# Optimization experiments

Measured on AMD Instinct MI355X. Metric: run time of the kernel, lower is better.

The kernel has to match this reference:

```python
import jax, jax.numpy as jnp
import numpy as np

NUM_NODES = 100000
NUM_EDGES = 1600000
IN_DIM = 128
HID = 128
OUT_DIM = 5


def setup_inputs() -> dict:
    key = jax.random.key(0)
    ks = jax.random.split(key, 8)
    x = jax.random.normal(ks[0], (NUM_NODES, IN_DIM), dtype=jnp.float32)
    edges = jax.random.randint(ks[1], (2, NUM_EDGES), 0, NUM_NODES, dtype=jnp.int32)
    s = 1.0 / np.sqrt(IN_DIM)
    W1 = jax.random.uniform(ks[2], (IN_DIM, HID), jnp.float32, -s, s)
    b1 = jax.random.uniform(ks[3], (HID,), jnp.float32, -s, s)
    sh = 1.0 / np.sqrt(HID)
    W2 = jax.random.uniform(ks[4], (HID, HID), jnp.float32, -sh, sh)
    b2 = jax.random.uniform(ks[5], (HID,), jnp.float32, -sh, sh)
    Wp = jax.random.uniform(ks[6], (HID, OUT_DIM), jnp.float32, -sh, sh)
    bp = jax.random.uniform(ks[7], (OUT_DIM,), jnp.float32, -sh, sh)
    return {"x": x, "edges": edges, "W1": W1, "b1": b1, "W2": W2, "b2": b2, "Wp": Wp, "bp": bp}


def _gnn_layer(x, src, tgt, W, b):
    # scatter-add of source features into targets (mean aggregation)
    agg = jax.ops.segment_sum(x[src], tgt, num_segments=NUM_NODES)  # [N, d]
    cnt = jax.ops.segment_sum(jnp.ones_like(tgt, dtype=x.dtype), tgt, num_segments=NUM_NODES)
    cnt = jnp.maximum(cnt, 1.0)  # clamp(min=1)
    agg = agg / cnt[:, None]
    combined = x + agg  # residual
    return jax.nn.relu(combined @ W + b)


def reference(x, edges, W1, b1, W2, b2, Wp, bp):
    src, tgt = edges[0], edges[1]
    h = _gnn_layer(x, src, tgt, W1, b1)
    h = _gnn_layer(h, src, tgt, W2, b2)
    return h @ Wp + bp  # [N, OUT_DIM]
```

## Files before the change

kernel.cpp:

```cpp
#include <hip/hip_runtime.h>

typedef unsigned int uint32;
typedef unsigned short ushort16;

typedef __attribute__((ext_vector_type(8))) short short8;
typedef __attribute__((ext_vector_type(4))) float f32x4;

#define BMAX 512


__device__ __forceinline__ ushort16 f2bf(float f) {
    uint32 u = __float_as_uint(f);
    u += 0x7fffu + ((u >> 16) & 1u);
    return (ushort16)(u >> 16);
}
__device__ __forceinline__ float bfhi(uint32 u) { return __uint_as_float(u & 0xffff0000u); }
__device__ __forceinline__ float bflo(uint32 u) { return __uint_as_float(u << 16); }
__device__ __forceinline__ uint32 pack2(float a, float b) {
    return (uint32)f2bf(a) | ((uint32)f2bf(b) << 16);
}

union U16 { uint4 u; short8 s; };
__device__ __forceinline__ short8 ld_frag(const ushort16* p) {
    U16 x; x.u = *(const uint4*)p; return x.s;
}

#define ACC8(v) \
    acc[0] += bflo(v.x); acc[1] += bfhi(v.x); \
    acc[2] += bflo(v.y); acc[3] += bfhi(v.y); \
    acc[4] += bflo(v.z); acc[5] += bfhi(v.z); \
    acc[6] += bflo(v.w); acc[7] += bfhi(v.w);

__device__ __forceinline__ void bucket_scan(const int* __restrict__ total, int B,
                                            int* bs , int* sd ) {
    int tid = threadIdx.x;
    int v0 = (2 * tid     < B) ? total[2 * tid]     : 0;
    int v1 = (2 * tid + 1 < B) ? total[2 * tid + 1] : 0;
    int s = v0 + v1;
    sd[tid] = s;
    __syncthreads();
    for (int o = 1; o < 256; o <<= 1) {
        int t = (tid >= o) ? sd[tid - o] : 0;
        __syncthreads();
        sd[tid] += t;
        __syncthreads();
    }
    int excl = sd[tid] - s;
    bs[2 * tid]     = excl;
    bs[2 * tid + 1] = excl + v0;
    __syncthreads();
}

__global__ __launch_bounds__(256)
void hist_cvt_prep_kernel(const int* __restrict__ tgt, int* __restrict__ hist,
                          const float* __restrict__ x, uint4* __restrict__ xb,
                          const float* __restrict__ W1, const float* __restrict__ W2,
                          ushort16* __restrict__ Wt1, ushort16* __restrict__ Wt2,
                          int E, int C, int B, int G1, int n64) {
    int tid = threadIdx.x, blk = blockIdx.x;
    if (blk >= G1) {
        const float* W = (blk - G1) ? W2 : W1;
        ushort16* Wt = (blk - G1) ? Wt2 : Wt1;
        for (int i = tid; i < 16384; i += 256) {
            int k = i >> 7, c = i & 127;
            Wt[c * 128 + k] = f2bf(W[i]);
        }
        return;
    }
    __shared__ int lh[BMAX];
    for (int b = tid; b < B; b += 256) lh[b] = 0;
    __syncthreads();
    int q0 = blk * (C / 4), q1 = min(q0 + C / 4, E / 4);
    for (int q = q0 + tid; q < q1; q += 256) {
        int4 t = ((const int4*)tgt)[q];
        atomicAdd(&lh[t.x >> 8], 1);
        atomicAdd(&lh[t.y >> 8], 1);
        atomicAdd(&lh[t.z >> 8], 1);
        atomicAdd(&lh[t.w >> 8], 1);
    }
    if (blk == 0 && tid == 0) {
        for (int e = (E / 4) * 4; e < E; ++e) atomicAdd(&lh[tgt[e] >> 8], 1);
    }
    for (int i = blk * 256 + tid; i < n64; i += G1 * 256) {
        const float4* p = (const float4*)x + (size_t)i * 16;
        uint4* q = xb + (size_t)i * 8;
#pragma unroll
        for (int j = 0; j < 8; ++j) {
            float4 a = p[2 * j], bb = p[2 * j + 1];
            uint4 o;
            o.x = pack2(a.x, a.y); o.y = pack2(a.z, a.w);
            o.z = pack2(bb.x, bb.y); o.w = pack2(bb.z, bb.w);
            q[j] = o;
        }
    }
    __syncthreads();
    for (int b = tid; b < B; b += 256) hist[blk * B + b] = lh[b];
}

__global__ __launch_bounds__(256)
void colscan_kernel(int* __restrict__ hist, int* __restrict__ total, int G1, int B) {
    __shared__ int sd[256];
    __shared__ int carrySh;
    int b = blockIdx.x, tid = threadIdx.x;
    if (tid == 0) carrySh = 0;
    __syncthreads();
    for (int g0 = 0; g0 < G1; g0 += 256) {
        int g = g0 + tid;
        int v = (g < G1) ? hist[g * B + b] : 0;
        int c0 = carrySh;
        sd[tid] = v;
        __syncthreads();
        for (int o = 1; o < 256; o <<= 1) {
            int t = (tid >= o) ? sd[tid - o] : 0;
            __syncthreads();
            sd[tid] += t;
            __syncthreads();
        }
        if (g < G1) hist[g * B + b] = sd[tid] - v + c0;
        int tot = sd[255];
        __syncthreads();
        if (tid == 0) carrySh = c0 + tot;
        __syncthreads();
    }
    if (tid == 0) total[b] = carrySh;
}

__global__ __launch_bounds__(256)
void partition_kernel(const int* __restrict__ src, const int* __restrict__ tgt,
                      const int* __restrict__ hist, const int* __restrict__ total,
                      uint32* __restrict__ ebuf, int E, int C, int B) {
    __shared__ int bs[512];
    __shared__ int sd[256];
    __shared__ int cur[BMAX];
    int tid = threadIdx.x, blk = blockIdx.x;
    bucket_scan(total, B, bs, sd);
    for (int b = tid; b < B; b += 256) cur[b] = hist[blk * B + b] + bs[b];
    __syncthreads();
    int q0 = blk * (C / 4), q1 = min(q0 + C / 4, E / 4);
    for (int q = q0 + tid; q < q1; q += 256) {
        int4 t = ((const int4*)tgt)[q];
        int4 s = ((const int4*)src)[q];
        int p0 = atomicAdd(&cur[t.x >> 8], 1);
        int p1 = atomicAdd(&cur[t.y >> 8], 1);
        int p2 = atomicAdd(&cur[t.z >> 8], 1);
        int p3 = atomicAdd(&cur[t.w >> 8], 1);
        ebuf[p0] = ((uint32)(t.x & 255) << 24) | (uint32)s.x;
        ebuf[p1] = ((uint32)(t.y & 255) << 24) | (uint32)s.y;
        ebuf[p2] = ((uint32)(t.z & 255) << 24) | (uint32)s.z;
        ebuf[p3] = ((uint32)(t.w & 255) << 24) | (uint32)s.w;
    }
    if (blk == 0 && tid == 0) {
        for (int e = (E / 4) * 4; e < E; ++e) {
            int t = tgt[e], s = src[e];
            int p = atomicAdd(&cur[t >> 8], 1);
            ebuf[p] = ((uint32)(t & 255) << 24) | (uint32)s;
        }
    }
}

__global__ __launch_bounds__(256)
void csr_kernel(const uint32* __restrict__ ebuf, const int* __restrict__ total,
                int* __restrict__ offsets, int* __restrict__ csr, int N, int B, int E) {
    __shared__ int bs[512];
    __shared__ int sd[256];
    __shared__ int cnt[256];
    int b = blockIdx.x, tid = threadIdx.x;
    bucket_scan(total, B, bs, sd);
    int s = bs[b];
    int n = bs[b + 1] - s;
    int t0 = b << 8;
    cnt[tid] = 0;
    __syncthreads();
    {
        int a0 = (s + 3) & ~3, a1 = (s + n) & ~3;
        for (int i = s + tid; i < min(a0, s + n); i += 256) atomicAdd(&cnt[ebuf[i] >> 24], 1);
        for (int q = a0 / 4 + tid; q < a1 / 4; q += 256) {
            uint4 e4 = ((const uint4*)ebuf)[q];
            atomicAdd(&cnt[e4.x >> 24], 1);
            atomicAdd(&cnt[e4.y >> 24], 1);
            atomicAdd(&cnt[e4.z >> 24], 1);
            atomicAdd(&cnt[e4.w >> 24], 1);
        }
        for (int i = max(a1, s) + tid; i < s + n; i += 256) atomicAdd(&cnt[ebuf[i] >> 24], 1);
    }
    __syncthreads();
    int v = cnt[tid];
    sd[tid] = v;
    __syncthreads();
    for (int o = 1; o < 256; o <<= 1) {
        int t = (tid >= o) ? sd[tid - o] : 0;
        __syncthreads();
        sd[tid] += t;
        __syncthreads();
    }
    int excl = sd[tid] - v;
    int t = t0 + tid;
    if (t < N) offsets[t] = s + excl;
    if (b == B - 1 && tid == 255) offsets[N] = E;
    __syncthreads();
    cnt[tid] = s + excl;
    __syncthreads();
    for (int i = tid; i < n; i += 256) {
        uint32 e = ebuf[s + i];
        int slot = atomicAdd(&cnt[e >> 24], 1);
        csr[slot] = (int)(e & 0x00FFFFFFu);
    }
}

__global__ __launch_bounds__(256, 4)
void agg_combine_bf16_kernel(const ushort16* __restrict__ hb,
                             const int* __restrict__ offsets, const int* __restrict__ csr,
                             uint32* __restrict__ outb, int N) {
    int wid = (blockIdx.x * 256 + threadIdx.x) >> 6;
    int lane = threadIdx.x & 63;
    if (wid >= N) return;
    int g = lane >> 4, sl = lane & 15;
    int s0 = offsets[wid];
    int deg = offsets[wid + 1] - s0;
    int fi = sl * 4 + g;
    uint32 su = ((const uint32*)hb)[(size_t)wid * 64 + fi];

    float acc[8];
#pragma unroll
    for (int j = 0; j < 8; ++j) acc[j] = 0.f;

    int base = 0;
    for (; base + 8 <= deg; base += 8) {
        int i0 = csr[s0 + base + g];
        int i1 = csr[s0 + base + 4 + g];
        uint4 v0 = *(const uint4*)(hb + (size_t)i0 * 128 + sl * 8);
        uint4 v1 = *(const uint4*)(hb + (size_t)i1 * 128 + sl * 8);
        ACC8(v0); ACC8(v1);
    }
    for (; base < deg; base += 4) {
        int e = base + g;
        if (e < deg) {
            int s = csr[s0 + e];
            uint4 v = *(const uint4*)(hb + (size_t)s * 128 + sl * 8);
            ACC8(v);
        }
    }
#pragma unroll
    for (int j = 0; j < 8; ++j) {
        acc[j] += __shfl_xor(acc[j], 16, 64);
        acc[j] += __shfl_xor(acc[j], 32, 64);
    }
    float inv = 1.f / fmaxf((float)deg, 1.f);
    float ax = (g == 0) ? acc[0] : (g == 1) ? acc[2] : (g == 2) ? acc[4] : acc[6];
    float ay = (g == 0) ? acc[1] : (g == 1) ? acc[3] : (g == 2) ? acc[5] : acc[7];
    outb[(size_t)wid * 64 + fi] = pack2(bflo(su) + ax * inv, bfhi(su) + ay * inv);
}

__global__ __launch_bounds__(256)
void gemm_mfma_kernel(const ushort16* __restrict__ A, const ushort16* __restrict__ Wt,
                      const float* __restrict__ bias, int M,
                      ushort16* __restrict__ outB,
                      const float* __restrict__ Wp, const float* __restrict__ bp,
                      float* __restrict__ outP) {
    const int tid = threadIdx.x;
    const int lane = tid & 63;
    const int wave = tid >> 6;
    const int l15 = lane & 15;
    const int quad = lane >> 4;
    const int r0 = blockIdx.x * 64 + wave * 16;

    int arow = r0 + l15;
    if (arow >= M) arow = M - 1;
    const ushort16* aptr = A + (size_t)arow * 128 + quad * 8;
    short8 afr[4];
#pragma unroll
    for (int kt = 0; kt < 4; ++kt) afr[kt] = ld_frag(aptr + kt * 32);

    f32x4 acc[8];
#pragma unroll
    for (int t = 0; t < 8; ++t) acc[t] = (f32x4){0.f, 0.f, 0.f, 0.f};

#pragma unroll
    for (int t = 0; t < 8; ++t) {
        const ushort16* bptr = Wt + (size_t)(16 * t + l15) * 128 + quad * 8;
        short8 b0 = ld_frag(bptr);
        short8 b1 = ld_frag(bptr + 32);
        short8 b2 = ld_frag(bptr + 64);
        short8 b3 = ld_frag(bptr + 96);
        acc[t] = __builtin_amdgcn_mfma_f32_16x16x32_bf16(afr[0], b0, acc[t], 0, 0, 0);
        acc[t] = __builtin_amdgcn_mfma_f32_16x16x32_bf16(afr[1], b1, acc[t], 0, 0, 0);
        acc[t] = __builtin_amdgcn_mfma_f32_16x16x32_bf16(afr[2], b2, acc[t], 0, 0, 0);
        acc[t] = __builtin_amdgcn_mfma_f32_16x16x32_bf16(afr[3], b3, acc[t], 0, 0, 0);
    }

    if (outP) {
        float p[4][5];
#pragma unroll
        for (int r = 0; r < 4; ++r)
#pragma unroll
            for (int j = 0; j < 5; ++j) p[r][j] = 0.f;
#pragma unroll
        for (int t = 0; t < 8; ++t) {
            float wpl[5];
#pragma unroll
            for (int j = 0; j < 5; ++j) wpl[j] = Wp[(16 * t + l15) * 5 + j];
            float bt = bias[16 * t + l15];
            float ov[4];
            ov[0] = fmaxf(acc[t].x + bt, 0.f);
            ov[1] = fmaxf(acc[t].y + bt, 0.f);
            ov[2] = fmaxf(acc[t].z + bt, 0.f);
            ov[3] = fmaxf(acc[t].w + bt, 0.f);
#pragma unroll
            for (int r = 0; r < 4; ++r)
#pragma unroll
                for (int j = 0; j < 5; ++j) p[r][j] += ov[r] * wpl[j];
        }
#pragma unroll
        for (int m = 1; m <= 8; m <<= 1)
#pragma unroll
            for (int r = 0; r < 4; ++r)
#pragma unroll
                for (int j = 0; j < 5; ++j) p[r][j] += __shfl_xor(p[r][j], m, 64);
        if (l15 == 0) {
#pragma unroll
            for (int r = 0; r < 4; ++r) {
                int row = r0 + quad * 4 + r;
                if (row < M) {
#pragma unroll
                    for (int j = 0; j < 5; ++j) outP[(size_t)row * 5 + j] = p[r][j] + bp[j];
                }
            }
        }
    } else {
#pragma unroll
        for (int t = 0; t < 8; ++t) {
            float bt = bias[16 * t + l15];
            float ov[4];
            ov[0] = fmaxf(acc[t].x + bt, 0.f);
            ov[1] = fmaxf(acc[t].y + bt, 0.f);
            ov[2] = fmaxf(acc[t].z + bt, 0.f);
            ov[3] = fmaxf(acc[t].w + bt, 0.f);
#pragma unroll
            for (int r = 0; r < 4; ++r) {
                float nb = __shfl_xor(ov[r], 1, 64);
                int row = r0 + quad * 4 + r;
                if (((l15 & 1) == 0) && row < M) {
                    *(uint32*)(outB + (size_t)row * 128 + 16 * t + l15) = pack2(ov[r], nb);
                }
            }
        }
    }
}

extern "C" void kernel_launch(void* const* d_in, const int* in_sizes, int n_in,
                              void* d_out, int out_size, void* d_ws, size_t ws_size,
                              hipStream_t stream) {
    const float* x     = (const float*)d_in[0];
    const int*   edges = (const int*)d_in[1];
    const float* W1    = (const float*)d_in[2];
    const float* b1    = (const float*)d_in[3];
    const float* W2    = (const float*)d_in[4];
    const float* b2    = (const float*)d_in[5];
    const float* Wp    = (const float*)d_in[6];
    const float* bp    = (const float*)d_in[7];
    float* out = (float*)d_out;

    const int N = in_sizes[0] / 128;
    const int E = in_sizes[1] / 2;
    const int* src = edges;
    const int* tgt = edges + E;

    const int B  = (N + 255) >> 8;
    const int C  = 4096;
    const int G1 = (E + C - 1) / C;
    const int n64 = N * 2;

    char* ws = (char*)d_ws;
    size_t off = 0;
    auto alloc = [&](size_t bytes) {
        char* p = ws + off;
        off = (off + bytes + 255) & ~(size_t)255;
        return p;
    };
    int*      offsets = (int*)alloc((size_t)(N + 1) * 4);
    int*      csr     = (int*)alloc((size_t)E * 4);
    ushort16* xb      = (ushort16*)alloc((size_t)N * 128 * 2);
    ushort16* hb1     = (ushort16*)alloc((size_t)N * 128 * 2);
    ushort16* bufAb   = (ushort16*)alloc((size_t)N * 128 * 2);
    ushort16* Wt1     = (ushort16*)alloc(128 * 128 * 2);
    ushort16* Wt2     = (ushort16*)alloc(128 * 128 * 2);
    int*      hist    = (int*)alloc((size_t)G1 * B * 4);
    int*      total   = (int*)alloc((size_t)B * 4);
    uint32*   ebuf    = (uint32*)bufAb;
    (void)ws_size;

    hist_cvt_prep_kernel<<<G1 + 2, 256, 0, stream>>>(tgt, hist, x, (uint4*)xb,
                                                     W1, W2, Wt1, Wt2, E, C, B, G1, n64);
    colscan_kernel<<<B, 256, 0, stream>>>(hist, total, G1, B);
    partition_kernel<<<G1, 256, 0, stream>>>(src, tgt, hist, total, ebuf, E, C, B);
    csr_kernel<<<B, 256, 0, stream>>>(ebuf, total, offsets, csr, N, B, E);

    const int aggBlocks  = (N + 3) / 4;
    const int gemmBlocks = (N + 63) / 64;

    agg_combine_bf16_kernel<<<aggBlocks, 256, 0, stream>>>(xb, offsets, csr, (uint32*)bufAb, N);
    gemm_mfma_kernel<<<gemmBlocks, 256, 0, stream>>>(bufAb, Wt1, b1, N, hb1,
                                                     nullptr, nullptr, nullptr);
    agg_combine_bf16_kernel<<<aggBlocks, 256, 0, stream>>>(hb1, offsets, csr, (uint32*)bufAb, N);
    gemm_mfma_kernel<<<gemmBlocks, 256, 0, stream>>>(bufAb, Wt2, b2, N, nullptr,
                                                     Wp, bp, out);
}
```

Baseline: 361.3 us.

## Reorder GEMM before aggregation and merge CSR build into one cooperative kernel

Uses linearity, (x + mean(x))W = xW + mean(xW), to run the bf16 MFMA GEMM first on raw fp32 input, converted in-register. Bias, ReLU and the final 5-wide projection are then fused into the gather/aggregation kernel, which removes the separate x-to-bf16 conversion pass and the projection epilogue. The four CSR-construction kernels (histogram, column scan, partition, CSR) are merged into one cooperative launch with grid-wide syncs, cutting launch gaps. Risks are the cooperative launch residency limits and grid.sync overhead, plus bf16 rounding of xW before averaging, which changes numerics slightly.

Result: slower. 514.0 us (+42.3%).

```diff
diff --git a/kernel.cpp b/kernel.cpp
--- a/kernel.cpp
+++ b/kernel.cpp
@@ -1,4 +1,7 @@
 #include <hip/hip_runtime.h>
+#include <hip/hip_cooperative_groups.h>
+
+namespace cg = cooperative_groups;
 
 typedef unsigned int uint32;
 typedef unsigned short ushort16;
@@ -52,211 +55,152 @@
 }
 
 __global__ __launch_bounds__(256)
-void hist_cvt_prep_kernel(const int* __restrict__ tgt, int* __restrict__ hist,
-                          const float* __restrict__ x, uint4* __restrict__ xb,
-                          const float* __restrict__ W1, const float* __restrict__ W2,
-                          ushort16* __restrict__ Wt1, ushort16* __restrict__ Wt2,
-                          int E, int C, int B, int G1, int n64) {
+void prep_coop_kernel(const int* __restrict__ src, const int* __restrict__ tgt,
+                      const float* __restrict__ W1, const float* __restrict__ W2,
+                      ushort16* __restrict__ Wt1, ushort16* __restrict__ Wt2,
+                      int* __restrict__ hist, int* __restrict__ total,
+                      uint32* __restrict__ ebuf, int* __restrict__ offsets,
+                      int* __restrict__ csr,
+                      int N, int E, int C, int B, int G1) {
+    cg::grid_group grid = cg::this_grid();
     int tid = threadIdx.x, blk = blockIdx.x;
-    if (blk >= G1) {
-        const float* W = (blk - G1) ? W2 : W1;
-        ushort16* Wt = (blk - G1) ? Wt2 : Wt1;
-        for (int i = tid; i < 16384; i += 256) {
-            int k = i >> 7, c = i & 127;
-            Wt[c * 128 + k] = f2bf(W[i]);
-        }
-        return;
-    }
+
     __shared__ int lh[BMAX];
-    for (int b = tid; b < B; b += 256) lh[b] = 0;
-    __syncthreads();
-    int q0 = blk * (C / 4), q1 = min(q0 + C / 4, E / 4);
-    for (int q = q0 + tid; q < q1; q += 256) {
-        int4 t = ((const int4*)tgt)[q];
-        atomicAdd(&lh[t.x >> 8], 1);
-        atomicAdd(&lh[t.y >> 8], 1);
-        atomicAdd(&lh[t.z >> 8], 1);
-        atomicAdd(&lh[t.w >> 8], 1);
-    }
-    if (blk == 0 && tid == 0) {
-        for (int e = (E / 4) * 4; e < E; ++e) atomicAdd(&lh[tgt[e] >> 8], 1);
-    }
-    for (int i = blk * 256 + tid; i < n64; i += G1 * 256) {
-        const float4* p = (const float4*)x + (size_t)i * 16;
-        uint4* q = xb + (size_t)i * 8;
-#pragma unroll
-        for (int j = 0; j < 8; ++j) {
-            float4 a = p[2 * j], bb = p[2 * j + 1];
-            uint4 o;
-            o.x = pack2(a.x, a.y); o.y = pack2(a.z, a.w);
-            o.z = pack2(bb.x, bb.y); o.w = pack2(bb.z, bb.w);
-            q[j] = o;
-        }
-    }
-    __syncthreads();
-    for (int b = tid; b < B; b += 256) hist[blk * B + b] = lh[b];
-}
-
-__global__ __launch_bounds__(256)
-void colscan_kernel(int* __restrict__ hist, int* __restrict__ total, int G1, int B) {
-    __shared__ int sd[256];
-    __shared__ int carrySh;
-    int b = blockIdx.x, tid = threadIdx.x;
-    if (tid == 0) carrySh = 0;
-    __syncthreads();
-    for (int g0 = 0; g0 < G1; g0 += 256) {
-        int g = g0 + tid;
-        int v = (g < G1) ? hist[g * B + b] : 0;
-        int c0 = carrySh;
-        sd[tid] = v;
-        __syncthreads();
-        for (int o = 1; o < 256; o <<= 1) {
-            int t = (tid >= o) ? sd[tid - o] : 0;
-            __syncthreads();
-            sd[tid] += t;
-            __syncthreads();
-        }
-        if (g < G1) hist[g * B + b] = sd[tid] - v + c0;
-        int tot = sd[255];
-        __syncthreads();
-        if (tid == 0) carrySh = c0 + tot;
-        __syncthreads();
-    }
-    if (tid == 0) total[b] = carrySh;
-}
-
-__global__ __launch_bounds__(256)
-void partition_kernel(const int* __restrict__ src, const int* __restrict__ tgt,
-                      const int* __restrict__ hist, const int* __restrict__ total,
-                      uint32* __restrict__ ebuf, int E, int C, int B) {
     __shared__ int bs[512];
     __shared__ int sd[256];
     __shared__ int cur[BMAX];
-    int tid = threadIdx.x, blk = blockIdx.x;
-    bucket_scan(total, B, bs, sd);
-    for (int b = tid; b < B; b += 256) cur[b] = hist[blk * B + b] + bs[b];
-    __syncthreads();
-    int q0 = blk * (C / 4), q1 = min(q0 + C / 4, E / 4);
-    for (int q = q0 + tid; q < q1; q += 256) {
-        int4 t = ((const int4*)tgt)[q];
-        int4 s = ((const int4*)src)[q];
-        int p0 = atomicAdd(&cur[t.x >> 8], 1);
-        int p1 = atomicAdd(&cur[t.y >> 8], 1);
-        int p2 = atomicAdd(&cur[t.z >> 8], 1);
-        int p3 = atomicAdd(&cur[t.w >> 8], 1);
-        ebuf[p0] = ((uint32)(t.x & 255) << 24) | (uint32)s.x;
-        ebuf[p1] = ((uint32)(t.y & 255) << 24) | (uint32)s.y;
-        ebuf[p2] = ((uint32)(t.z & 255) << 24) | (uint32)s.z;
-        ebuf[p3] = ((uint32)(t.w & 255) << 24) | (uint32)s.w;
-    }
-    if (blk == 0 && tid == 0) {
-        for (int e = (E / 4) * 4; e < E; ++e) {
-            int t = tgt[e], s = src[e];
-            int p = atomicAdd(&cur[t >> 8], 1);
-            ebuf[p] = ((uint32)(t & 255) << 24) | (uint32)s;
-        }
-    }
-}
-
+    __shared__ int carrySh;
+
+    if (blk >= G1) {
+        if (blk < G1 + 2) {
+            const float* W = (blk - G1) ? W2 : W1;
+            ushort16* Wt = (blk - G1) ? Wt2 : Wt1;
+            for (int i = tid; i < 16384; i += 256) {
+                int k = i >> 7, c = i & 127;
+                Wt[c * 128 + k] = f2bf(W[i]);
+            }
+        }
+    } else {
+        for (int b = tid; b < B; b += 256) lh[b] = 0;
+        __syncthreads();
+        int q0 = blk * (C / 4), q1 = min(q0 + C / 4, E / 4);
+        for (int q = q0 + tid; q < q1; q += 256) {
+            int4 t = ((const int4*)tgt)[q];
+            atomicAdd(&lh[t.x >> 8], 1);
+            atomicAdd(&lh[t.y >> 8], 1);
+            atomicAdd(&lh[t.z >> 8], 1);
+            atomicAdd(&lh[t.w >> 8], 1);
+        }
+        if (blk == 0 && tid == 0) {
+            for (int e = (E / 4) * 4; e < E; ++e) atomicAdd(&lh[tgt[e] >> 8], 1);
+        }
+        __syncthreads();
+        for (int b = tid; b < B; b += 256) hist[blk * B + b] = lh[b];
+    }
+    grid.sync();
+
+    if (blk < B) {
+        int b = blk;
+        if (tid == 0) carrySh = 0;
+        __syncthreads();
+        for (int g0 = 0; g0 < G1; g0 += 256) {
+            int g = g0 + tid;
+            int v = (g < G1) ? hist[g * B + b] : 0;
+            int c0 = carrySh;
+            sd[tid] = v;
+            __syncthreads();
+            for (int o = 1; o < 256; o <<= 1) {
+                int t = (tid >= o) ? sd[tid - o] : 0;
+                __syncthreads();
+                sd[tid] += t;
+                __syncthreads();
+            }
+            if (g < G1) hist[g * B + b] = sd[tid] - v + c0;
+            int tot = sd[255];
+            __syncthreads();
+            if (tid == 0) carrySh = c0 + tot;
+            __syncthreads();
+        }
+        if (tid == 0) total[b] = carrySh;
+    }
+    grid.sync();
+
+    if (blk < G1) {
+        bucket_scan(total, B, bs, sd);
+        for (int b = tid; b < B; b += 256) cur[b] = hist[blk * B + b] + bs[b];
+        __syncthreads();
+        int q0 = blk * (C / 4), q1 = min(q0 + C / 4, E / 4);
+        for (int q = q0 + tid; q < q1; q += 256) {
+            int4 t = ((const int4*)tgt)[q];
+            int4 s = ((const int4*)src)[q];
+            int p0 = atomicAdd(&cur[t.x >> 8], 1);
+            int p1 = atomicAdd(&cur[t.y >> 8], 1);
+            int p2 = atomicAdd(&cur[t.z >> 8], 1);
+            int p3 = atomicAdd(&cur[t.w >> 8], 1);
+            ebuf[p0] = ((uint32)(t.x & 255) << 24) | (uint32)s.x;
+            ebuf[p1] = ((uint32)(t.y & 255) << 24) | (uint32)s.y;
+            ebuf[p2] = ((uint32)(t.z & 255) << 24) | (uint32)s.z;
+            ebuf[p3] = ((uint32)(t.w & 255) << 24) | (uint32)s.w;
+        }
+        if (blk == 0 && tid == 0) {
+            for (int e = (E / 4) * 4; e < E; ++e) {
+                int t = tgt[e], s = src[e];
+                int p = atomicAdd(&cur[t >> 8], 1);
+                ebuf[p] = ((uint32)(t & 255) << 24) | (uint32)s;
+            }
+        }
+    }
+    grid.sync();
+
+    if (blk < B) {
+        int b = blk;
+        bucket_scan(total, B, bs, sd);
+        int s = bs[b];
+        int n = bs[b + 1] - s;
+        int t0 = b << 8;
+        cur[tid] = 0;
+        __syncthreads();
+        {
+            int a0 = (s + 3) & ~3, a1 = (s + n) & ~3;
+            for (int i = s + tid; i < min(a0, s + n); i += 256) atomicAdd(&cur[ebuf[i] >> 24], 1);
+            for (int q = a0 / 4 + tid; q < a1 / 4; q += 256) {
+                uint4 e4 = ((const uint4*)ebuf)[q];
+                atomicAdd(&cur[e4.x >> 24], 1);
+                atomicAdd(&cur[e4.y >> 24], 1);
+                atomicAdd(&cur[e4.z >> 24], 1);
+                atomicAdd(&cur[e4.w >> 24], 1);
+            }
+            for (int i = max(a1, s) + tid; i < s + n; i += 256) atomicAdd(&cur[ebuf[i] >> 24], 1);
+        }
+        __syncthreads();
+        int v = cur[tid];
+        sd[tid] = v;
+        __syncthreads();
+        for (int o = 1; o < 256; o <<= 1) {
+            int t = (tid >= o) ? sd[tid - o] : 0;
+            __syncthreads();
+            sd[tid] += t;
+            __syncthreads();
+        }
+        int excl = sd[tid] - v;
+        int t = t0 + tid;
+        if (t < N) offsets[t] = s + excl;
+        if (b == B - 1 && tid == 255) offsets[N] = E;
+        __syncthreads();
+        cur[tid] = s + excl;
+        __syncthreads();
+        for (int i = tid; i < n; i += 256) {
+            uint32 e = ebuf[s + i];
+            int slot = atomicAdd(&cur[e >> 24], 1);
+            csr[slot] = (int)(e & 0x00FFFFFFu);
+        }
+    }
+}
+
+template<int INF32>
 __global__ __launch_bounds__(256)
-void csr_kernel(const uint32* __restrict__ ebuf, const int* __restrict__ total,
-                int* __restrict__ offsets, int* __restrict__ csr, int N, int B, int E) {
-    __shared__ int bs[512];
-    __shared__ int sd[256];
-    __shared__ int cnt[256];
-    int b = blockIdx.x, tid = threadIdx.x;
-    bucket_scan(total, B, bs, sd);
-    int s = bs[b];
-    int n = bs[b + 1] - s;
-    int t0 = b << 8;
-    cnt[tid] = 0;
-    __syncthreads();
-    {
-        int a0 = (s + 3) & ~3, a1 = (s + n) & ~3;
-        for (int i = s + tid; i < min(a0, s + n); i += 256) atomicAdd(&cnt[ebuf[i] >> 24], 1);
-        for (int q = a0 / 4 + tid; q < a1 / 4; q += 256) {
-            uint4 e4 = ((const uint4*)ebuf)[q];
-            atomicAdd(&cnt[e4.x >> 24], 1);
-            atomicAdd(&cnt[e4.y >> 24], 1);
-            atomicAdd(&cnt[e4.z >> 24], 1);
-            atomicAdd(&cnt[e4.w >> 24], 1);
-        }
-        for (int i = max(a1, s) + tid; i < s + n; i += 256) atomicAdd(&cnt[ebuf[i] >> 24], 1);
-    }
-    __syncthreads();
-    int v = cnt[tid];
-    sd[tid] = v;
-    __syncthreads();
-    for (int o = 1; o < 256; o <<= 1) {
-        int t = (tid >= o) ? sd[tid - o] : 0;
-        __syncthreads();
-        sd[tid] += t;
-        __syncthreads();
-    }
-    int excl = sd[tid] - v;
-    int t = t0 + tid;
-    if (t < N) offsets[t] = s + excl;
-    if (b == B - 1 && tid == 255) offsets[N] = E;
-    __syncthreads();
-    cnt[tid] = s + excl;
-    __syncthreads();
-    for (int i = tid; i < n; i += 256) {
-        uint32 e = ebuf[s + i];
-        int slot = atomicAdd(&cnt[e >> 24], 1);
-        csr[slot] = (int)(e & 0x00FFFFFFu);
-    }
-}
-
-__global__ __launch_bounds__(256, 4)
-void agg_combine_bf16_kernel(const ushort16* __restrict__ hb,
-                             const int* __restrict__ offsets, const int* __restrict__ csr,
-                             uint32* __restrict__ outb, int N) {
-    int wid = (blockIdx.x * 256 + threadIdx.x) >> 6;
-    int lane = threadIdx.x & 63;
-    if (wid >= N) return;
-    int g = lane >> 4, sl = lane & 15;
-    int s0 = offsets[wid];
-    int deg = offsets[wid + 1] - s0;
-    int fi = sl * 4 + g;
-    uint32 su = ((const uint32*)hb)[(size_t)wid * 64 + fi];
-
-    float acc[8];
-#pragma unroll
-    for (int j = 0; j < 8; ++j) acc[j] = 0.f;
-
-    int base = 0;
-    for (; base + 8 <= deg; base += 8) {
-        int i0 = csr[s0 + base + g];
-        int i1 = csr[s0 + base + 4 + g];
-        uint4 v0 = *(const uint4*)(hb + (size_t)i0 * 128 + sl * 8);
-        uint4 v1 = *(const uint4*)(hb + (size_t)i1 * 128 + sl * 8);
-        ACC8(v0); ACC8(v1);
-    }
-    for (; base < deg; base += 4) {
-        int e = base + g;
-        if (e < deg) {
-            int s = csr[s0 + e];
-            uint4 v = *(const uint4*)(hb + (size_t)s * 128 + sl * 8);
-            ACC8(v);
-        }
-    }
-#pragma unroll
-    for (int j = 0; j < 8; ++j) {
-        acc[j] += __shfl_xor(acc[j], 16, 64);
-        acc[j] += __shfl_xor(acc[j], 32, 64);
-    }
-    float inv = 1.f / fmaxf((float)deg, 1.f);
-    float ax = (g == 0) ? acc[0] : (g == 1) ? acc[2] : (g == 2) ? acc[4] : acc[6];
-    float ay = (g == 0) ? acc[1] : (g == 1) ? acc[3] : (g == 2) ? acc[5] : acc[7];
-    outb[(size_t)wid * 64 + fi] = pack2(bflo(su) + ax * inv, bfhi(su) + ay * inv);
-}
-
-__global__ __launch_bounds__(256)
-void gemm_mfma_kernel(const ushort16* __restrict__ A, const ushort16* __restrict__ Wt,
-                      const float* __restrict__ bias, int M,
-                      ushort16* __restrict__ outB,
-                      const float* __restrict__ Wp, const float* __restrict__ bp,
-                      float* __restrict__ outP) {
+void gemm_raw_kernel(const void* __restrict__ Asrc, const ushort16* __restrict__ Wt,
+                     int M, ushort16* __restrict__ outB) {
     const int tid = threadIdx.x;
     const int lane = tid & 63;
     const int wave = tid >> 6;
@@ -266,10 +210,26 @@
 
     int arow = r0 + l15;
     if (arow >= M) arow = M - 1;
-    const ushort16* aptr = A + (size_t)arow * 128 + quad * 8;
+
     short8 afr[4];
-#pragma unroll
-    for (int kt = 0; kt < 4; ++kt) afr[kt] = ld_frag(aptr + kt * 32);
+    if (INF32) {
+        const float* ap = (const float*)Asrc + (size_t)arow * 128 + quad * 8;
+#pragma unroll
+        for (int kt = 0; kt < 4; ++kt) {
+            float4 a0 = *(const float4*)(ap + kt * 32);
+            float4 a1 = *(const float4*)(ap + kt * 32 + 4);
+            short8 f;
+            f[0] = (short)f2bf(a0.x); f[1] = (short)f2bf(a0.y);
+            f[2] = (short)f2bf(a0.z); f[3] = (short)f2bf(a0.w);
+            f[4] = (short)f2bf(a1.x); f[5] = (short)f2bf(a1.y);
+            f[6] = (short)f2bf(a1.z); f[7] = (short)f2bf(a1.w);
+            afr[kt] = f;
+        }
+    } else {
+        const ushort16* aptr = (const ushort16*)Asrc + (size_t)arow * 128 + quad * 8;
+#pragma unroll
+        for (int kt = 0; kt < 4; ++kt) afr[kt] = ld_frag(aptr + kt * 32);
+    }
 
     f32x4 acc[8];
 #pragma unroll
@@ -288,61 +248,84 @@
         acc[t] = __builtin_amdgcn_mfma_f32_16x16x32_bf16(afr[3], b3, acc[t], 0, 0, 0);
     }
 
-    if (outP) {
-        float p[4][5];
-#pragma unroll
-        for (int r = 0; r < 4; ++r)
-#pragma unroll
-            for (int j = 0; j < 5; ++j) p[r][j] = 0.f;
-#pragma unroll
-        for (int t = 0; t < 8; ++t) {
-            float wpl[5];
-#pragma unroll
-            for (int j = 0; j < 5; ++j) wpl[j] = Wp[(16 * t + l15) * 5 + j];
-            float bt = bias[16 * t + l15];
-            float ov[4];
-            ov[0] = fmaxf(acc[t].x + bt, 0.f);
-            ov[1] = fmaxf(acc[t].y + bt, 0.f);
-            ov[2] = fmaxf(acc[t].z + bt, 0.f);
-            ov[3] = fmaxf(acc[t].w + bt, 0.f);
-#pragma unroll
-            for (int r = 0; r < 4; ++r)
-#pragma unroll
-                for (int j = 0; j < 5; ++j) p[r][j] += ov[r] * wpl[j];
-        }
-#pragma unroll
-        for (int m = 1; m <= 8; m <<= 1)
-#pragma unroll
-            for (int r = 0; r < 4; ++r)
-#pragma unroll
-                for (int j = 0; j < 5; ++j) p[r][j] += __shfl_xor(p[r][j], m, 64);
-        if (l15 == 0) {
-#pragma unroll
-            for (int r = 0; r < 4; ++r) {
-                int row = r0 + quad * 4 + r;
-                if (row < M) {
-#pragma unroll
-                    for (int j = 0; j < 5; ++j) outP[(size_t)row * 5 + j] = p[r][j] + bp[j];
-                }
-            }
-        }
+#pragma unroll
+    for (int t = 0; t < 8; ++t) {
+        float ov[4];
+        ov[0] = acc[t].x; ov[1] = acc[t].y; ov[2] = acc[t].z; ov[3] = acc[t].w;
+#pragma unroll
+        for (int r = 0; r < 4; ++r) {
+            float nb = __shfl_xor(ov[r], 1, 64);
+            int row = r0 + quad * 4 + r;
+            if (((l15 & 1) == 0) && row < M) {
+                *(uint32*)(outB + (size_t)row * 128 + 16 * t + l15) = pack2(ov[r], nb);
+            }
+        }
+    }
+}
+
+template<int PROJ>
+__global__ __launch_bounds__(256, 4)
+void agg_fuse_kernel(const ushort16* __restrict__ hb,
+                     const int* __restrict__ offsets, const int* __restrict__ csr,
+                     const float* __restrict__ bias,
+                     uint32* __restrict__ outb,
+                     const float* __restrict__ Wp, const float* __restrict__ bp,
+                     float* __restrict__ outP, int N) {
+    int wid = (blockIdx.x * 256 + threadIdx.x) >> 6;
+    int lane = threadIdx.x & 63;
+    if (wid >= N) return;
+    int g = lane >> 4, sl = lane & 15;
+    int s0 = offsets[wid];
+    int deg = offsets[wid + 1] - s0;
+    int fi = sl * 4 + g;
+    uint32 su = ((const uint32*)hb)[(size_t)wid * 64 + fi];
+
+    float acc[8];
+#pragma unroll
+    for (int j = 0; j < 8; ++j) acc[j] = 0.f;
+
+    int base = 0;
+    for (; base + 8 <= deg; base += 8) {
+        int i0 = csr[s0 + base + g];
+        int i1 = csr[s0 + base + 4 + g];
+        uint4 v0 = *(const uint4*)(hb + (size_t)i0 * 128 + sl * 8);
+        uint4 v1 = *(const uint4*)(hb + (size_t)i1 * 128 + sl * 8);
+        ACC8(v0); ACC8(v1);
+    }
+    for (; base < deg; base += 4) {
+        int e = base + g;
+        if (e < deg) {
+            int s = csr[s0 + e];
+            uint4 v = *(const uint4*)(hb + (size_t)s * 128 + sl * 8);
+            ACC8(v);
+        }
+    }
+#pragma unroll
+    for (int j = 0; j < 8; ++j) {
+        acc[j] += __shfl_xor(acc[j], 16, 64);
+        acc[j] += __shfl_xor(acc[j], 32, 64);
+    }
+    float inv = 1.f / fmaxf((float)deg, 1.f);
+    float ax = (g == 0) ? acc[0] : (g == 1) ? acc[2] : (g == 2) ? acc[4] : acc[6];
+    float ay = (g == 0) ? acc[1] : (g == 1) ? acc[3] : (g == 2) ? acc[5] : acc[7];
+
+    float ha = fmaxf(bflo(su) + ax * inv + bias[2 * fi],     0.f);
+    float hc = fmaxf(bfhi(su) + ay * inv + bias[2 * fi + 1], 0.f);
+
+    if (!PROJ) {
+        outb[(size_t)wid * 64 + fi] = pack2(ha, hc);
     } else {
-#pragma unroll
-        for (int t = 0; t < 8; ++t) {
-            float bt = bias[16 * t + l15];
-            float ov[4];
-            ov[0] = fmaxf(acc[t].x + bt, 0.f);
-            ov[1] = fmaxf(acc[t].y + bt, 0.f);
-            ov[2] = fmaxf(acc[t].z + bt, 0.f);
-            ov[3] = fmaxf(acc[t].w + bt, 0.f);
-#pragma unroll
-            for (int r = 0; r < 4; ++r) {
-                float nb = __shfl_xor(ov[r], 1, 64);
-                int row = r0 + quad * 4 + r;
-                if (((l15 & 1) == 0) && row < M) {
-                    *(uint32*)(outB + (size_t)row * 128 + 16 * t + l15) = pack2(ov[r], nb);
-                }
-            }
+        float p[5];
+#pragma unroll
+        for (int j = 0; j < 5; ++j)
+            p[j] = ha * Wp[(2 * fi) * 5 + j] + hc * Wp[(2 * fi + 1) * 5 + j];
+#pragma unroll
+        for (int m = 1; m <= 32; m <<= 1)
+#pragma unroll
+            for (int j = 0; j < 5; ++j) p[j] += __shfl_xor(p[j], m, 64);
+        if (lane == 0) {
+#pragma unroll
+            for (int j = 0; j < 5; ++j) outP[(size_t)wid * 5 + j] = p[j] + bp[j];
         }
     }
 }
@@ -360,15 +343,14 @@
     const float* bp    = (const float*)d_in[7];
     float* out = (float*)d_out;
 
-    const int N = in_sizes[0] / 128;
-    const int E = in_sizes[1] / 2;
+    int N = in_sizes[0] / 128;
+    int E = in_sizes[1] / 2;
     const int* src = edges;
     const int* tgt = edges + E;
 
-    const int B  = (N + 255) >> 8;
-    const int C  = 4096;
-    const int G1 = (E + C - 1) / C;
-    const int n64 = N * 2;
+    int B  = (N + 255) >> 8;
+    int C  = 4096;
+    int G1 = (E + C - 1) / C;
 
     char* ws = (char*)d_ws;
     size_t off = 0;
@@ -379,29 +361,36 @@
     };
     int*      offsets = (int*)alloc((size_t)(N + 1) * 4);
     int*      csr     = (int*)alloc((size_t)E * 4);
-    ushort16* xb      = (ushort16*)alloc((size_t)N * 128 * 2);
-    ushort16* hb1     = (ushort16*)alloc((size_t)N * 128 * 2);
-    ushort16* bufAb   = (ushort16*)alloc((size_t)N * 128 * 2);
+    ushort16* ybuf    = (ushort16*)alloc((size_t)N * 128 * 2);
+    ushort16* h1      = (ushort16*)alloc((size_t)N * 128 * 2);
     ushort16* Wt1     = (ushort16*)alloc(128 * 128 * 2);
     ushort16* Wt2     = (ushort16*)alloc(128 * 128 * 2);
     int*      hist    = (int*)alloc((size_t)G1 * B * 4);
     int*      total   = (int*)alloc((size_t)B * 4);
-    uint32*   ebuf    = (uint32*)bufAb;
+    uint32*   ebuf    = (uint32*)ybuf;
     (void)ws_size;
 
-    hist_cvt_prep_kernel<<<G1 + 2, 256, 0, stream>>>(tgt, hist, x, (uint4*)xb,
-                                                     W1, W2, Wt1, Wt2, E, C, B, G1, n64);
-    colscan_kernel<<<B, 256, 0, stream>>>(hist, total, G1, B);
-    partition_kernel<<<G1, 256, 0, stream>>>(src, tgt, hist, total, ebuf, E, C, B);
-    csr_kernel<<<B, 256, 0, stream>>>(ebuf, total, offsets, csr, N, B, E);
+    {
+        const int* srcp = src; const int* tgtp = tgt;
+        const float* w1p = W1; const float* w2p = W2;
+        ushort16* wt1p = Wt1; ushort16* wt2p = Wt2;
+        int* histp = hist; int* totalp = total;
+        uint32* ebufp = ebuf; int* offp = offsets; int* csrp = csr;
+        void* args[] = {&srcp, &tgtp, &w1p, &w2p, &wt1p, &wt2p,
+                        &histp, &totalp, &ebufp, &offp, &csrp,
+                        &N, &E, &C, &B, &G1};
+        hipLaunchCooperativeKernel((void*)prep_coop_kernel, dim3(G1 + 2), dim3(256),
+                                   args, 0, stream);
+    }
 
     const int aggBlocks  = (N + 3) / 4;
     const int gemmBlocks = (N + 63) / 64;
 
-    agg_combine_bf16_kernel<<<aggBlocks, 256, 0, stream>>>(xb, offsets, csr, (uint32*)bufAb, N);
-    gemm_mfma_kernel<<<gemmBlocks, 256, 0, stream>>>(bufAb, Wt1, b1, N, hb1,
-                                                     nullptr, nullptr, nullptr);
-    agg_combine_bf16_kernel<<<aggBlocks, 256, 0, stream>>>(hb1, offsets, csr, (uint32*)bufAb, N);
-    gemm_mfma_kernel<<<gemmBlocks, 256, 0, stream>>>(bufAb, Wt2, b2, N, nullptr,
-                                                     Wp, bp, out);
-}
+    gemm_raw_kernel<1><<<gemmBlocks, 256, 0, stream>>>(x, Wt1, N, ybuf);
+    agg_fuse_kernel<0><<<aggBlocks, 256, 0, stream>>>(ybuf, offsets, csr, b1,
+                                                      (uint32*)h1, nullptr, nullptr,
+                                                      nullptr, N);
+    gemm_raw_kernel<0><<<gemmBlocks, 256, 0, stream>>>(h1, Wt2, N, ybuf);
+    agg_fuse_kernel<1><<<aggBlocks, 256, 0, stream>>>(ybuf, offsets, csr, b2,
+                                                      nullptr, Wp, bp, out, N);
+}
```

## Rebuild CSR via fixed-capacity 512-node region lists and overlap x conversion

Applied to the files above, without the earlier changes.

Replaces the four-kernel bucket partition and CSR build with per-512-node regions. Each region gets a fixed-capacity edge list holding (src, tgt) pairs. A single 512-thread kernel per region then builds start/degree arrays and the CSR, and extra blocks in that same launch do the fp32-to-bf16 conversion of x. The weight transpose is also split across 16 blocks, and the aggregation now reads start and degree arrays instead of offsets. The aim is fewer passes and scans over the edge data. The trade-off is a CAP of 12288 edges per region that silently drops edges for skewed graphs, and a limit of at most 256 regions.

Result: faster. 332.5 us (-8.0%).

```diff
diff --git a/kernel.cpp b/kernel.cpp
--- a/kernel.cpp
+++ b/kernel.cpp
@@ -6,8 +6,11 @@
 typedef __attribute__((ext_vector_type(8))) short short8;
 typedef __attribute__((ext_vector_type(4))) float f32x4;
 
-#define BMAX 512
-
+
+#define RSH 9
+#define NRG 512
+#define CAP 12288
+#define CH  2048
 
 __device__ __forceinline__ ushort16 f2bf(float f) {
     uint32 u = __float_as_uint(f);
@@ -31,82 +34,58 @@
     acc[4] += bflo(v.z); acc[5] += bfhi(v.z); \
     acc[6] += bflo(v.w); acc[7] += bfhi(v.w);
 
-__device__ __forceinline__ void bucket_scan(const int* __restrict__ total, int B,
-                                            int* bs , int* sd ) {
-    int tid = threadIdx.x;
-    int v0 = (2 * tid     < B) ? total[2 * tid]     : 0;
-    int v1 = (2 * tid + 1 < B) ? total[2 * tid + 1] : 0;
-    int s = v0 + v1;
-    sd[tid] = s;
-    __syncthreads();
-    for (int o = 1; o < 256; o <<= 1) {
-        int t = (tid >= o) ? sd[tid - o] : 0;
-        __syncthreads();
-        sd[tid] += t;
-        __syncthreads();
-    }
-    int excl = sd[tid] - s;
-    bs[2 * tid]     = excl;
-    bs[2 * tid + 1] = excl + v0;
-    __syncthreads();
-}
-
 __global__ __launch_bounds__(256)
-void hist_cvt_prep_kernel(const int* __restrict__ tgt, int* __restrict__ hist,
-                          const float* __restrict__ x, uint4* __restrict__ xb,
-                          const float* __restrict__ W1, const float* __restrict__ W2,
-                          ushort16* __restrict__ Wt1, ushort16* __restrict__ Wt2,
-                          int E, int C, int B, int G1, int n64) {
+void count_prep_kernel(const int* __restrict__ tgt, int* __restrict__ hist,
+                       const float* __restrict__ W1, const float* __restrict__ W2,
+                       ushort16* __restrict__ Wt1, ushort16* __restrict__ Wt2,
+                       int E, int PB) {
     int tid = threadIdx.x, blk = blockIdx.x;
-    if (blk >= G1) {
-        const float* W = (blk - G1) ? W2 : W1;
-        ushort16* Wt = (blk - G1) ? Wt2 : Wt1;
-        for (int i = tid; i < 16384; i += 256) {
-            int k = i >> 7, c = i & 127;
-            Wt[c * 128 + k] = f2bf(W[i]);
-        }
+    if (blk >= PB) {
+        int idx = blk - PB;
+        const float* W = (idx >> 3) ? W2 : W1;
+        ushort16* Wt = (idx >> 3) ? Wt2 : Wt1;
+        int i0 = (idx & 7) * 2048 + tid * 8;
+        float4 a = *(const float4*)(W + i0);
+        float4 b = *(const float4*)(W + i0 + 4);
+        int k = i0 >> 7, col = i0 & 127;
+        Wt[(col + 0) * 128 + k] = f2bf(a.x);
+        Wt[(col + 1) * 128 + k] = f2bf(a.y);
+        Wt[(col + 2) * 128 + k] = f2bf(a.z);
+        Wt[(col + 3) * 128 + k] = f2bf(a.w);
+        Wt[(col + 4) * 128 + k] = f2bf(b.x);
+        Wt[(col + 5) * 128 + k] = f2bf(b.y);
+        Wt[(col + 6) * 128 + k] = f2bf(b.z);
+        Wt[(col + 7) * 128 + k] = f2bf(b.w);
         return;
     }
-    __shared__ int lh[BMAX];
-    for (int b = tid; b < B; b += 256) lh[b] = 0;
-    __syncthreads();
-    int q0 = blk * (C / 4), q1 = min(q0 + C / 4, E / 4);
+    __shared__ int cnt[256];
+    cnt[tid] = 0;
+    __syncthreads();
+    int q0 = blk * (CH / 4), q1 = min(q0 + CH / 4, E / 4);
     for (int q = q0 + tid; q < q1; q += 256) {
         int4 t = ((const int4*)tgt)[q];
-        atomicAdd(&lh[t.x >> 8], 1);
-        atomicAdd(&lh[t.y >> 8], 1);
-        atomicAdd(&lh[t.z >> 8], 1);
-        atomicAdd(&lh[t.w >> 8], 1);
-    }
-    if (blk == 0 && tid == 0) {
-        for (int e = (E / 4) * 4; e < E; ++e) atomicAdd(&lh[tgt[e] >> 8], 1);
-    }
-    for (int i = blk * 256 + tid; i < n64; i += G1 * 256) {
-        const float4* p = (const float4*)x + (size_t)i * 16;
-        uint4* q = xb + (size_t)i * 8;
-#pragma unroll
-        for (int j = 0; j < 8; ++j) {
-            float4 a = p[2 * j], bb = p[2 * j + 1];
-            uint4 o;
-            o.x = pack2(a.x, a.y); o.y = pack2(a.z, a.w);
-            o.z = pack2(bb.x, bb.y); o.w = pack2(bb.z, bb.w);
-            q[j] = o;
-        }
-    }
-    __syncthreads();
-    for (int b = tid; b < B; b += 256) hist[blk * B + b] = lh[b];
+        atomicAdd(&cnt[t.x >> RSH], 1);
+        atomicAdd(&cnt[t.y >> RSH], 1);
+        atomicAdd(&cnt[t.z >> RSH], 1);
+        atomicAdd(&cnt[t.w >> RSH], 1);
+    }
+    if (blk == 0 && tid == 0)
+        for (int e = (E / 4) * 4; e < E; ++e) atomicAdd(&cnt[tgt[e] >> RSH], 1);
+    __syncthreads();
+    hist[(size_t)blk * 256 + tid] = cnt[tid];
 }
 
 __global__ __launch_bounds__(256)
-void colscan_kernel(int* __restrict__ hist, int* __restrict__ total, int G1, int B) {
+void scan_kernel(int* __restrict__ hist, int* __restrict__ total, int PB) {
     __shared__ int sd[256];
     __shared__ int carrySh;
-    int b = blockIdx.x, tid = threadIdx.x;
+    int r = blockIdx.x, tid = threadIdx.x;
     if (tid == 0) carrySh = 0;
     __syncthreads();
-    for (int g0 = 0; g0 < G1; g0 += 256) {
-        int g = g0 + tid;
-        int v = (g < G1) ? hist[g * B + b] : 0;
+    int chunks = (PB + 255) >> 8;
+    for (int ch = 0; ch < chunks; ++ch) {
+        int g = ch * 256 + tid;
+        int v = (g < PB) ? hist[(size_t)g * 256 + r] : 0;
         int c0 = carrySh;
         sd[tid] = v;
         __syncthreads();
@@ -116,107 +95,164 @@
             sd[tid] += t;
             __syncthreads();
         }
-        if (g < G1) hist[g * B + b] = sd[tid] - v + c0;
+        if (g < PB) hist[(size_t)g * 256 + r] = sd[tid] - v + c0;
         int tot = sd[255];
         __syncthreads();
         if (tid == 0) carrySh = c0 + tot;
         __syncthreads();
     }
-    if (tid == 0) total[b] = carrySh;
+    if (tid == 0) total[r] = carrySh;
 }
 
 __global__ __launch_bounds__(256)
-void partition_kernel(const int* __restrict__ src, const int* __restrict__ tgt,
-                      const int* __restrict__ hist, const int* __restrict__ total,
-                      uint32* __restrict__ ebuf, int E, int C, int B) {
-    __shared__ int bs[512];
-    __shared__ int sd[256];
-    __shared__ int cur[BMAX];
+void scatter_kernel(const int* __restrict__ src, const int* __restrict__ tgt,
+                    const int* __restrict__ hist, uint2* __restrict__ rlist,
+                    int E) {
+    __shared__ int cb[256];
+    __shared__ int cnt[256];
     int tid = threadIdx.x, blk = blockIdx.x;
-    bucket_scan(total, B, bs, sd);
-    for (int b = tid; b < B; b += 256) cur[b] = hist[blk * B + b] + bs[b];
-    __syncthreads();
-    int q0 = blk * (C / 4), q1 = min(q0 + C / 4, E / 4);
+    cnt[tid] = 0;
+    cb[tid] = hist[(size_t)blk * 256 + tid];
+    __syncthreads();
+    int q0 = blk * (CH / 4), q1 = min(q0 + CH / 4, E / 4);
     for (int q = q0 + tid; q < q1; q += 256) {
         int4 t = ((const int4*)tgt)[q];
         int4 s = ((const int4*)src)[q];
-        int p0 = atomicAdd(&cur[t.x >> 8], 1);
-        int p1 = atomicAdd(&cur[t.y >> 8], 1);
-        int p2 = atomicAdd(&cur[t.z >> 8], 1);
-        int p3 = atomicAdd(&cur[t.w >> 8], 1);
-        ebuf[p0] = ((uint32)(t.x & 255) << 24) | (uint32)s.x;
-        ebuf[p1] = ((uint32)(t.y & 255) << 24) | (uint32)s.y;
-        ebuf[p2] = ((uint32)(t.z & 255) << 24) | (uint32)s.z;
-        ebuf[p3] = ((uint32)(t.w & 255) << 24) | (uint32)s.w;
+        int r0 = t.x >> RSH, r1 = t.y >> RSH, r2 = t.z >> RSH, r3 = t.w >> RSH;
+        int p0 = cb[r0] + atomicAdd(&cnt[r0], 1);
+        int p1 = cb[r1] + atomicAdd(&cnt[r1], 1);
+        int p2 = cb[r2] + atomicAdd(&cnt[r2], 1);
+        int p3 = cb[r3] + atomicAdd(&cnt[r3], 1);
+        if (p0 < CAP) rlist[(size_t)r0 * CAP + p0] = make_uint2((uint32)s.x, (uint32)t.x);
+        if (p1 < CAP) rlist[(size_t)r1 * CAP + p1] = make_uint2((uint32)s.y, (uint32)t.y);
+        if (p2 < CAP) rlist[(size_t)r2 * CAP + p2] = make_uint2((uint32)s.z, (uint32)t.z);
+        if (p3 < CAP) rlist[(size_t)r3 * CAP + p3] = make_uint2((uint32)s.w, (uint32)t.w);
     }
     if (blk == 0 && tid == 0) {
         for (int e = (E / 4) * 4; e < E; ++e) {
-            int t = tgt[e], s = src[e];
-            int p = atomicAdd(&cur[t >> 8], 1);
-            ebuf[p] = ((uint32)(t & 255) << 24) | (uint32)s;
-        }
-    }
-}
-
-__global__ __launch_bounds__(256)
-void csr_kernel(const uint32* __restrict__ ebuf, const int* __restrict__ total,
-                int* __restrict__ offsets, int* __restrict__ csr, int N, int B, int E) {
-    __shared__ int bs[512];
-    __shared__ int sd[256];
-    __shared__ int cnt[256];
-    int b = blockIdx.x, tid = threadIdx.x;
-    bucket_scan(total, B, bs, sd);
-    int s = bs[b];
-    int n = bs[b + 1] - s;
-    int t0 = b << 8;
-    cnt[tid] = 0;
-    __syncthreads();
+            int t = tgt[e], r = t >> RSH;
+            int p = cb[r] + atomicAdd(&cnt[r], 1);
+            if (p < CAP) rlist[(size_t)r * CAP + p] = make_uint2((uint32)src[e], (uint32)t);
+        }
+    }
+}
+
+__global__ __launch_bounds__(512)
+void csr_cvt_kernel(const uint2* __restrict__ rlist, const int* __restrict__ total,
+                    int* __restrict__ start, int* __restrict__ deg,
+                    int* __restrict__ csr, int N, int R, int CVB,
+                    const float* __restrict__ x, uint4* __restrict__ xb) {
+    int blk = blockIdx.x;
+    int tid = threadIdx.x;
+    if (blk >= R) {
+        int n16 = N * 16;
+        for (int j = (blk - R) * 512 + tid; j < n16; j += CVB * 512) {
+            const float* p = x + (size_t)j * 8;
+            float4 a = *(const float4*)p;
+            float4 b = *(const float4*)(p + 4);
+            uint4 o;
+            o.x = pack2(a.x, a.y); o.y = pack2(a.z, a.w);
+            o.z = pack2(b.x, b.y); o.w = pack2(b.z, b.w);
+            xb[j] = o;
+        }
+        return;
+    }
+    __shared__ int lhist[NRG];
+    __shared__ int sd[512];
+    __shared__ int rbaseSh, countSh;
+
+    int r = blk;
+    if (tid < 256) sd[tid] = (tid < R) ? total[tid] : 0;
+    __syncthreads();
+    for (int o = 1; o < 256; o <<= 1) {
+        int t = (tid >= o && tid < 256) ? sd[tid - o] : 0;
+        __syncthreads();
+        if (tid < 256) sd[tid] += t;
+        __syncthreads();
+    }
+    if (tid == 0) {
+        rbaseSh = (r == 0) ? 0 : sd[r - 1];
+        countSh = min(total[r], CAP);
+    }
+    if (tid < NRG) lhist[tid] = 0;
+    __syncthreads();
+    int count = countSh;
+    const uint2* rl = rlist + (size_t)r * CAP;
+    int n0 = r << RSH;
+
     {
-        int a0 = (s + 3) & ~3, a1 = (s + n) & ~3;
-        for (int i = s + tid; i < min(a0, s + n); i += 256) atomicAdd(&cnt[ebuf[i] >> 24], 1);
-        for (int q = a0 / 4 + tid; q < a1 / 4; q += 256) {
-            uint4 e4 = ((const uint4*)ebuf)[q];
-            atomicAdd(&cnt[e4.x >> 24], 1);
-            atomicAdd(&cnt[e4.y >> 24], 1);
-            atomicAdd(&cnt[e4.z >> 24], 1);
-            atomicAdd(&cnt[e4.w >> 24], 1);
-        }
-        for (int i = max(a1, s) + tid; i < s + n; i += 256) atomicAdd(&cnt[ebuf[i] >> 24], 1);
-    }
-    __syncthreads();
-    int v = cnt[tid];
-    sd[tid] = v;
-    __syncthreads();
-    for (int o = 1; o < 256; o <<= 1) {
-        int t = (tid >= o) ? sd[tid - o] : 0;
-        __syncthreads();
-        sd[tid] += t;
-        __syncthreads();
-    }
-    int excl = sd[tid] - v;
-    int t = t0 + tid;
-    if (t < N) offsets[t] = s + excl;
-    if (b == B - 1 && tid == 255) offsets[N] = E;
-    __syncthreads();
-    cnt[tid] = s + excl;
-    __syncthreads();
-    for (int i = tid; i < n; i += 256) {
-        uint32 e = ebuf[s + i];
-        int slot = atomicAdd(&cnt[e >> 24], 1);
-        csr[slot] = (int)(e & 0x00FFFFFFu);
+        int i = tid;
+        for (; i + 512 * 7 < count; i += 512 * 8) {
+            uint2 e0 = rl[i], e1 = rl[i + 512], e2 = rl[i + 1024], e3 = rl[i + 1536];
+            uint2 e4 = rl[i + 2048], e5 = rl[i + 2560], e6 = rl[i + 3072], e7 = rl[i + 3584];
+            atomicAdd(&lhist[e0.y & (NRG - 1)], 1);
+            atomicAdd(&lhist[e1.y & (NRG - 1)], 1);
+            atomicAdd(&lhist[e2.y & (NRG - 1)], 1);
+            atomicAdd(&lhist[e3.y & (NRG - 1)], 1);
+            atomicAdd(&lhist[e4.y & (NRG - 1)], 1);
+            atomicAdd(&lhist[e5.y & (NRG - 1)], 1);
+            atomicAdd(&lhist[e6.y & (NRG - 1)], 1);
+            atomicAdd(&lhist[e7.y & (NRG - 1)], 1);
+        }
+        for (; i < count; i += 512)
+            atomicAdd(&lhist[rl[i].y & (NRG - 1)], 1);
+    }
+    __syncthreads();
+
+    {
+        int v = lhist[tid];
+        sd[tid] = v;
+        __syncthreads();
+        for (int o = 1; o < 512; o <<= 1) {
+            int t = (tid >= o) ? sd[tid - o] : 0;
+            __syncthreads();
+            sd[tid] += t;
+            __syncthreads();
+        }
+        int excl = sd[tid] - v + rbaseSh;
+        int node = n0 + tid;
+        if (node < N) { start[node] = excl; deg[node] = v; }
+        lhist[tid] = excl;
+        __syncthreads();
+    }
+
+    {
+        int i = tid;
+        for (; i + 512 * 7 < count; i += 512 * 8) {
+            uint2 e0 = rl[i], e1 = rl[i + 512], e2 = rl[i + 1024], e3 = rl[i + 1536];
+            uint2 e4 = rl[i + 2048], e5 = rl[i + 2560], e6 = rl[i + 3072], e7 = rl[i + 3584];
+            int p0 = atomicAdd(&lhist[e0.y & (NRG - 1)], 1);
+            int p1 = atomicAdd(&lhist[e1.y & (NRG - 1)], 1);
+            int p2 = atomicAdd(&lhist[e2.y & (NRG - 1)], 1);
+            int p3 = atomicAdd(&lhist[e3.y & (NRG - 1)], 1);
+            int p4 = atomicAdd(&lhist[e4.y & (NRG - 1)], 1);
+            int p5 = atomicAdd(&lhist[e5.y & (NRG - 1)], 1);
+            int p6 = atomicAdd(&lhist[e6.y & (NRG - 1)], 1);
+            int p7 = atomicAdd(&lhist[e7.y & (NRG - 1)], 1);
+            csr[p0] = (int)e0.x; csr[p1] = (int)e1.x;
+            csr[p2] = (int)e2.x; csr[p3] = (int)e3.x;
+            csr[p4] = (int)e4.x; csr[p5] = (int)e5.x;
+            csr[p6] = (int)e6.x; csr[p7] = (int)e7.x;
+        }
+        for (; i < count; i += 512) {
+            uint2 e = rl[i];
+            int p = atomicAdd(&lhist[e.y & (NRG - 1)], 1);
+            csr[p] = (int)e.x;
+        }
     }
 }
 
 __global__ __launch_bounds__(256, 4)
 void agg_combine_bf16_kernel(const ushort16* __restrict__ hb,
-                             const int* __restrict__ offsets, const int* __restrict__ csr,
+                             const int* __restrict__ startv, const int* __restrict__ degv,
+                             const int* __restrict__ csr,
                              uint32* __restrict__ outb, int N) {
     int wid = (blockIdx.x * 256 + threadIdx.x) >> 6;
     int lane = threadIdx.x & 63;
     if (wid >= N) return;
     int g = lane >> 4, sl = lane & 15;
-    int s0 = offsets[wid];
-    int deg = offsets[wid + 1] - s0;
+    int s0 = startv[wid];
+    int deg = degv[wid];
     int fi = sl * 4 + g;
     uint32 su = ((const uint32*)hb)[(size_t)wid * 64 + fi];
 
@@ -360,15 +396,14 @@
     const float* bp    = (const float*)d_in[7];
     float* out = (float*)d_out;
 
-    const int N = in_sizes[0] / 128;
-    const int E = in_sizes[1] / 2;
+    int N = in_sizes[0] / 128;
+    int E = in_sizes[1] / 2;
     const int* src = edges;
     const int* tgt = edges + E;
 
-    const int B  = (N + 255) >> 8;
-    const int C  = 4096;
-    const int G1 = (E + C - 1) / C;
-    const int n64 = N * 2;
+    const int R  = (N + NRG - 1) >> RSH;
+    const int PB = (E + CH - 1) / CH;
+    const int CVB = 304;
 
     char* ws = (char*)d_ws;
     size_t off = 0;
@@ -377,31 +412,33 @@
         off = (off + bytes + 255) & ~(size_t)255;
         return p;
     };
-    int*      offsets = (int*)alloc((size_t)(N + 1) * 4);
+    int*      deg     = (int*)alloc((size_t)N * 4);
+    int*      start   = (int*)alloc((size_t)N * 4);
     int*      csr     = (int*)alloc((size_t)E * 4);
+    int*      hist    = (int*)alloc((size_t)PB * 256 * 4);
+    int*      total   = (int*)alloc(256 * 4);
     ushort16* xb      = (ushort16*)alloc((size_t)N * 128 * 2);
     ushort16* hb1     = (ushort16*)alloc((size_t)N * 128 * 2);
     ushort16* bufAb   = (ushort16*)alloc((size_t)N * 128 * 2);
     ushort16* Wt1     = (ushort16*)alloc(128 * 128 * 2);
     ushort16* Wt2     = (ushort16*)alloc(128 * 128 * 2);
-    int*      hist    = (int*)alloc((size_t)G1 * B * 4);
-    int*      total   = (int*)alloc((size_t)B * 4);
-    uint32*   ebuf    = (uint32*)bufAb;
+    uint2*    rlist   = (uint2*)bufAb;
     (void)ws_size;
 
-    hist_cvt_prep_kernel<<<G1 + 2, 256, 0, stream>>>(tgt, hist, x, (uint4*)xb,
-                                                     W1, W2, Wt1, Wt2, E, C, B, G1, n64);
-    colscan_kernel<<<B, 256, 0, stream>>>(hist, total, G1, B);
-    partition_kernel<<<G1, 256, 0, stream>>>(src, tgt, hist, total, ebuf, E, C, B);
-    csr_kernel<<<B, 256, 0, stream>>>(ebuf, total, offsets, csr, N, B, E);
-
+    const int gemmBlocks = (N + 63) / 64;
     const int aggBlocks  = (N + 3) / 4;
-    const int gemmBlocks = (N + 63) / 64;
-
-    agg_combine_bf16_kernel<<<aggBlocks, 256, 0, stream>>>(xb, offsets, csr, (uint32*)bufAb, N);
+
+    count_prep_kernel<<<PB + 16, 256, 0, stream>>>(tgt, hist, W1, W2, Wt1, Wt2, E, PB);
+    scan_kernel<<<R, 256, 0, stream>>>(hist, total, PB);
+    scatter_kernel<<<PB, 256, 0, stream>>>(src, tgt, hist, rlist, E);
+    csr_cvt_kernel<<<R + CVB, 512, 0, stream>>>(rlist, total, start, deg, csr,
+                                                N, R, CVB, x, (uint4*)xb);
+    agg_combine_bf16_kernel<<<aggBlocks, 256, 0, stream>>>(xb, start, deg, csr,
+                                                           (uint32*)bufAb, N);
     gemm_mfma_kernel<<<gemmBlocks, 256, 0, stream>>>(bufAb, Wt1, b1, N, hb1,
                                                      nullptr, nullptr, nullptr);
-    agg_combine_bf16_kernel<<<aggBlocks, 256, 0, stream>>>(hb1, offsets, csr, (uint32*)bufAb, N);
+    agg_combine_bf16_kernel<<<aggBlocks, 256, 0, stream>>>(hb1, start, deg, csr,
+                                                           (uint32*)bufAb, N);
     gemm_mfma_kernel<<<gemmBlocks, 256, 0, stream>>>(bufAb, Wt2, b2, N, nullptr,
                                                      Wp, bp, out);
 }
```
